# Performance work log

Measured on AMD Instinct MI355X. Metric: run time of the kernel, lower is better.

The kernel has to match this reference:

```python
import jax, jax.numpy as jnp
import numpy as np

N = 10000
E = 160000
IN_CH, HID, OUT = 14, 128, 4
HEADS = 8
NEG_SLOPE = 0.2


def setup_inputs() -> dict:
    key = jax.random.key(0)
    ks = jax.random.split(key, 16)
    glorot = lambda k, shape: jax.random.normal(k, shape, jnp.float32) * np.sqrt(2.0 / (shape[0] + shape[-1]))
    inp = {
        'x': jax.random.normal(ks[0], (N, IN_CH), jnp.float32),
        'edge_index': jax.random.randint(ks[1], (2, E), 0, N, jnp.int64),
        # layer 1: 14 -> 8 heads x 128, concat
        'W1': glorot(ks[2], (IN_CH, HEADS * HID)),
        'a_src1': glorot(ks[3], (HEADS, HID)),
        'a_dst1': glorot(ks[4], (HEADS, HID)),
        'b1': jnp.zeros((HEADS * HID,), jnp.float32),
        # layer 2: 1024 -> 8 heads x 128, concat
        'W2': glorot(ks[5], (HEADS * HID, HEADS * HID)),
        'a_src2': glorot(ks[6], (HEADS, HID)),
        'a_dst2': glorot(ks[7], (HEADS, HID)),
        'b2': jnp.zeros((HEADS * HID,), jnp.float32),
        # layer 3: 1024 -> 1 head x 4, mean (concat=False)
        'W3': glorot(ks[8], (HEADS * HID, OUT)),
        'a_src3': glorot(ks[9], (1, OUT)),
        'a_dst3': glorot(ks[10], (1, OUT)),
        'b3': jnp.zeros((OUT,), jnp.float32),
    }
    return inp


def gat_conv(x, src, dst, W, a_src, a_dst, b, heads, out_ch, concat):
    n = x.shape[0]
    h = (x @ W).reshape(n, heads, out_ch)                      # [N,H,C]
    al_s = jnp.sum(h * a_src, axis=-1)                         # [N,H]
    al_d = jnp.sum(h * a_dst, axis=-1)                         # [N,H]
    e = al_s[src] + al_d[dst]                                  # [E,H]
    e = jnp.where(e > 0, e, NEG_SLOPE * e)                     # LeakyReLU(0.2)
    # segment softmax over incoming edges of each dst node
    m = jax.ops.segment_max(e, dst, num_segments=n)
    ex = jnp.exp(e - m[dst])
    z = jax.ops.segment_sum(ex, dst, num_segments=n)
    alpha = ex / (z[dst] + 1e-16)                              # [E,H]
    out = jax.ops.segment_sum(h[src] * alpha[:, :, None], dst, num_segments=n)  # [N,H,C]
    out = out.reshape(n, heads * out_ch) if concat else out.mean(axis=1)
    return out + b


def reference(x, edge_index, W1, a_src1, a_dst1, b1, W2, a_src2, a_dst2, b2, W3, a_src3, a_dst3, b3):
    n = x.shape[0]
    # add self-loops (PyG GATConv default)
    loop = jnp.arange(n, dtype=edge_index.dtype)
    src = jnp.concatenate([edge_index[0], loop])
    dst = jnp.concatenate([edge_index[1], loop])
    # dropout layers are identity in eval mode
    h = gat_conv(x, src, dst, W1, a_src1, a_dst1, b1, HEADS, HID, True)
    h = jax.nn.relu(h)
    h = gat_conv(h, src, dst, W2, a_src2, a_dst2, b2, HEADS, HID, True)
    h = jax.nn.relu(h)
    h = gat_conv(h, src, dst, W3, a_src3, a_dst3, b3, 1, OUT, False)
    h = jax.nn.relu(h)
    return h
```

## Files before the change

kernel.cpp:

```cpp
#include <hip/hip_runtime.h>

typedef unsigned short ushort_t;
typedef unsigned int uint32;

#define N_NODES 10000
#define N_EDGES 160000
#define ET (N_NODES + N_EDGES)
#define HT 1024
#define HEADS 8
#define NEG 0.2f

#define O_FLAG     0
#define O_COUNTS   256
#define O_OFFS     (O_COUNTS + 40192)
#define O_SSORT    (O_OFFS + 40192)
#define O_ALS1     (O_SSORT + 680192)
#define O_ALD1     (O_ALS1 + 320000)
#define O_ALS2     (O_ALD1 + 320000)
#define O_ALD2     (O_ALS2 + 320000)
#define O_AL3S     O_ALS2
#define O_AL3D     (O_ALS2 + 40192)
#define O_H3       (O_ALS2 + 80384)
#define O_WVEC     (O_ALD2 + 320000)
#define O_W3F      (O_WVEC + 24576)
#define O_S3F      (O_W3F + 16384)
#define O_W2T      (O_S3F + 768)
#define O_BUFA     (O_W2T + 2097152)
#define O_BUFB     (O_BUFA + 20480000)

__device__ __forceinline__ float bf2f(ushort_t u){ return __uint_as_float(((uint32)u) << 16); }
__device__ __forceinline__ ushort_t f2bf(float f){
    uint32 x = __float_as_uint(f);
    return (ushort_t)((x + 0x7fffu + ((x >> 16) & 1u)) >> 16);
}
__device__ __forceinline__ void unpack2(uint32 u, float& lo, float& hi){
    lo = __uint_as_float(u << 16);
    hi = __uint_as_float(u & 0xffff0000u);
}

typedef __bf16 bf16x8 __attribute__((ext_vector_type(8)));
typedef float  f32x4  __attribute__((ext_vector_type(4)));

typedef const __attribute__((address_space(1))) uint32* gas1_u32;
typedef       __attribute__((address_space(3))) uint32* las3_u32;

__device__ __forceinline__ void gload_lds16(const void* g, void* l){
    __builtin_amdgcn_global_load_lds((gas1_u32)g, (las3_u32)l, 16, 0, 0);
}

__device__ __forceinline__ int probe_f32(const uint32* __restrict__ w){
    int cnt = 0;
    for (int i = 0; i < 256; i++){
        uint32 e = (w[i] >> 7) & 0xffu;
        cnt += (e >= 64u && e <= 160u) ? 1 : 0;
    }
    return (cnt > 200) ? 0 : 1;
}
__global__ void k_probe(const int* __restrict__ ei, const uint32* __restrict__ w1raw,
                        int* __restrict__ flags){
    if (threadIdx.x == 0){
        int nz = 0;
        for (int i = 0; i < 128; i++) nz |= ei[2*i + 1];
        flags[0] = (nz == 0) ? 1 : 0;
    }
    if (threadIdx.x == 1) flags[1] = probe_f32(w1raw);
}

__device__ __forceinline__ float cvt1(const void* p, int i, int f32){
    return f32 ? ((const float*)p)[i] : bf2f(((const ushort_t*)p)[i]);
}

struct CvtArgs {
    const void* vsrc[6];
    const void* w3src;
    const void* s3src[3];
};

__global__ __launch_bounds__(256) void k_setup(CvtArgs a, const void* __restrict__ W2,
                                               const int* __restrict__ flags,
                                               float* __restrict__ wvecF, float* __restrict__ W3F,
                                               float* __restrict__ s3F,
                                               int* __restrict__ counts,
                                               float* __restrict__ alS2, float* __restrict__ alD2,
                                               ushort_t* __restrict__ W2T){
    __shared__ ushort_t tile[32][33];
    int b = blockIdx.x, tid = threadIdx.x;
    int f32 = flags[1];
    if (b < 11){
        int g = b * 1024 + tid * 4;
        #pragma unroll
        for (int j = 0; j < 4; j++){
            int i = g + j;
            if (i < 6144) wvecF[i] = cvt1(a.vsrc[i >> 10], i & 1023, f32);
            else if (i < 10240) W3F[i - 6144] = cvt1(a.w3src, i - 6144, f32);
            else if (i < 10252){
                int off = i - 10240;
                s3F[(off >> 2) * 16 + (off & 3)] = cvt1(a.s3src[off >> 2], off & 3, f32);
            }
        }
    } else if (b < 21){
        int g = (b - 11) * 1024 + tid * 4;
        #pragma unroll
        for (int j = 0; j < 4; j++) if (g + j < N_NODES) counts[g + j] = 0;
    } else if (b < 178){
        int g = (b - 21) * 1024 + tid * 4;
        if (g < 80000){ *(float4*)(alS2 + g) = make_float4(0,0,0,0); }
        else if (g < 160000){ *(float4*)(alD2 + g - 80000) = make_float4(0,0,0,0); }
    } else {
        int t = b - 178;
        int bx = t & 31, by = t >> 5;
        int cx = tid & 31, ry = (tid >> 5) * 4;
        #pragma unroll
        for (int r = 0; r < 4; r++){
            size_t idx = (size_t)(by*32 + ry + r)*1024 + bx*32 + cx;
            tile[ry + r][cx] = f32 ? f2bf(((const float*)W2)[idx]) : ((const ushort_t*)W2)[idx];
        }
        __syncthreads();
        #pragma unroll
        for (int r = 0; r < 4; r++)
            W2T[(size_t)(bx*32 + ry + r)*1024 + by*32 + cx] = tile[cx][ry + r];
    }
}

__global__ __launch_bounds__(256) void k_extract_hist(const void* __restrict__ ei, const int* __restrict__ flags,
                                                      int* __restrict__ counts){
    int i = blockIdx.x * 256 + threadIdx.x;
    int is64 = flags[0];
    int d = -1;
    if (i < N_EDGES){
        d = is64 ? (int)((const long long*)ei)[N_EDGES + i] : ((const int*)ei)[N_EDGES + i];
    } else if (i < ET){
        d = i - N_EDGES;
    }
    if (d >= 0) atomicAdd(&counts[d], 1);
}

__global__ __launch_bounds__(1024) void k_scan(int* __restrict__ counts, int* __restrict__ offs, int n){
    __shared__ int wsum[16];
    __shared__ int running_s;
    int tid = threadIdx.x;
    int lane = tid & 63, wid = tid >> 6;
    if (tid == 0) running_s = 0;
    __syncthreads();
    for (int base = 0; base < n; base += 1024){
        int i = base + tid;
        int v = (i < n) ? counts[i] : 0;
        int x = v;
        #pragma unroll
        for (int d = 1; d < 64; d <<= 1){
            int t = __shfl_up(x, d, 64);
            if (lane >= d) x += t;
        }
        if (lane == 63) wsum[wid] = x;
        __syncthreads();
        if (wid == 0 && lane < 16){
            int w = wsum[lane];
            #pragma unroll
            for (int d = 1; d < 16; d <<= 1){
                int t = __shfl_up(w, d, 64);
                if (lane >= d) w += t;
            }
            wsum[lane] = w;
        }
        __syncthreads();
        int wprefix = (wid == 0) ? 0 : wsum[wid - 1];
        int run = running_s;
        int excl = run + wprefix + (x - v);
        if (i < n){ offs[i] = excl; counts[i] = excl; }
        __syncthreads();
        if (tid == 0) running_s = run + wsum[15];
        __syncthreads();
    }
    if (tid == 0) offs[n] = running_s;
}

__global__ __launch_bounds__(256) void k_scatter(const void* __restrict__ ei, const int* __restrict__ flags,
                                                 int* __restrict__ cursors, int* __restrict__ ssort){
    int i = blockIdx.x * 256 + threadIdx.x;
    if (i >= ET) return;
    int is64 = flags[0];
    int s, d;
    if (i < N_EDGES){
        if (is64){
            s = (int)((const long long*)ei)[i];
            d = (int)((const long long*)ei)[N_EDGES + i];
        } else {
            s = ((const int*)ei)[i];
            d = ((const int*)ei)[N_EDGES + i];
        }
    } else { s = i - N_EDGES; d = s; }
    int pos = atomicAdd(&cursors[d], 1);
    ssort[pos] = s;
}

__global__ __launch_bounds__(256) void k_gemm1f(const void* __restrict__ x, const void* __restrict__ W1,
                                                const int* __restrict__ flags,
                                                const float* __restrict__ wvecF,
                                                ushort_t* __restrict__ h1,
                                                float* __restrict__ alS, float* __restrict__ alD){
    __shared__ float w1s[14 * HT];
    int tid = threadIdx.x;
    int f32 = flags[1];
    if (f32){
        for (int i = tid * 4; i < 14 * HT; i += 1024)
            *(float4*)(w1s + i) = *(const float4*)((const float*)W1 + i);
    } else {
        for (int i = tid * 4; i < 14 * HT; i += 1024){
            uint2 u = *(const uint2*)((const ushort_t*)W1 + i);
            unpack2(u.x, w1s[i], w1s[i+1]);
            unpack2(u.y, w1s[i+2], w1s[i+3]);
        }
    }
    __syncthreads();
    int c0 = tid * 4;
    float4 sv = *(const float4*)(wvecF + c0);
    float4 dv = *(const float4*)(wvecF + 1024 + c0);
    int head = tid >> 5, l32 = tid & 31;
    #pragma unroll 1
    for (int n = blockIdx.x; n < N_NODES; n += 512){
        float a0=0.f, a1=0.f, a2=0.f, a3=0.f;
        #pragma unroll
        for (int k = 0; k < 14; k++){
            float xv = f32 ? ((const float*)x)[n*14 + k] : bf2f(((const ushort_t*)x)[n*14 + k]);
            float4 w = *(const float4*)(w1s + k*HT + c0);
            a0 += xv*w.x; a1 += xv*w.y; a2 += xv*w.z; a3 += xv*w.w;
        }
        uint2 o;
        o.x = (uint32)f2bf(a0) | ((uint32)f2bf(a1) << 16);
        o.y = (uint32)f2bf(a2) | ((uint32)f2bf(a3) << 16);
        *(uint2*)(h1 + (size_t)n*HT + c0) = o;
        float h0,h1v,h2,h3v;
        unpack2(o.x, h0, h1v); unpack2(o.y, h2, h3v);
        float s = h0*sv.x + h1v*sv.y + h2*sv.z + h3v*sv.w;
        float d = h0*dv.x + h1v*dv.y + h2*dv.z + h3v*dv.w;
        #pragma unroll
        for (int of = 16; of; of >>= 1){ s += __shfl_xor(s, of, 32); d += __shfl_xor(d, of, 32); }
        if (l32 == 0){ alS[n*HEADS + head] = s; alD[n*HEADS + head] = d; }
    }
}

__global__ __launch_bounds__(256) void k_gat_agg(const ushort_t* __restrict__ H, const float* __restrict__ alS,
                                                 const float* __restrict__ alD, const int* __restrict__ offs,
                                                 const int* __restrict__ srcs, const float* __restrict__ bias,
                                                 ushort_t* __restrict__ out){
    int tid = threadIdx.x;
    int wv = tid >> 6, lane = tid & 63;
    int n = blockIdx.x * 2 + (wv >> 1);
    int half = wv & 1;
    int beg = offs[n], end = offs[n+1];
    int head = half*4 + (lane >> 4);
    int slot = lane & 15;
    float ad = alD[n*HEADS + head];

    float m = -1e30f, z = 0.f;
    for (int c = beg; c < end; c += 64){
        int cn = min(64, end - c);
        int sreg = (lane < cn) ? srcs[c + lane] : 0;
        for (int p = slot; p < cn; p += 16){
            int s = __shfl(sreg, p, 64);
            float v = alS[s*HEADS + head] + ad;
            v = v > 0.f ? v : NEG*v;
            if (v > m){ z = z*__expf(m - v) + 1.f; m = v; }
            else z += __expf(v - m);
        }
    }
    #pragma unroll
    for (int o = 1; o < 16; o <<= 1){
        float m2 = __shfl_xor(m, o, 64);
        float z2 = __shfl_xor(z, o, 64);
        float nm = fmaxf(m, m2);
        z = z*__expf(m - nm) + z2*__expf(m2 - nm);
        m = nm;
    }
    float inv = 1.f / (z + 1e-16f);

    int ch0 = half*512 + lane*8;
    const ushort_t* Hc = H + ch0;
    float c0=0.f,c1=0.f,c2=0.f,c3=0.f,c4=0.f,c5=0.f,c6=0.f,c7=0.f;
    for (int c = beg; c < end; c += 64){
        int cn = min(64, end - c);
        int sreg = (lane < cn) ? srcs[c + lane] : 0;
        int j = 0;
        for (; j + 8 <= cn; j += 8){
            int s[8]; uint4 u[8]; float w[8];
            #pragma unroll
            for (int q = 0; q < 8; q++) s[q] = __shfl(sreg, j + q, 64);
            #pragma unroll
            for (int q = 0; q < 8; q++) u[q] = *(const uint4*)(Hc + (size_t)s[q]*HT);
            #pragma unroll
            for (int q = 0; q < 8; q++){
                float v = alS[s[q]*HEADS + head] + ad;
                v = v > 0.f ? v : NEG*v;
                w[q] = __expf(v - m) * inv;
            }
            #pragma unroll
            for (int q = 0; q < 8; q++){
                float f0,f1,f2,f3,f4,f5,f6,f7;
                unpack2(u[q].x,f0,f1); unpack2(u[q].y,f2,f3);
                unpack2(u[q].z,f4,f5); unpack2(u[q].w,f6,f7);
                c0+=w[q]*f0; c1+=w[q]*f1; c2+=w[q]*f2; c3+=w[q]*f3;
                c4+=w[q]*f4; c5+=w[q]*f5; c6+=w[q]*f6; c7+=w[q]*f7;
            }
        }
        for (; j < cn; j++){
            int s0 = __shfl(sreg, j, 64);
            uint4 u0 = *(const uint4*)(Hc + (size_t)s0*HT);
            float v0 = alS[s0*HEADS + head] + ad;
            v0 = v0 > 0.f ? v0 : NEG*v0;
            float w0 = __expf(v0 - m) * inv;
            float f0,f1,f2,f3,f4,f5,f6,f7;
            unpack2(u0.x,f0,f1); unpack2(u0.y,f2,f3); unpack2(u0.z,f4,f5); unpack2(u0.w,f6,f7);
            c0+=w0*f0; c1+=w0*f1; c2+=w0*f2; c3+=w0*f3;
            c4+=w0*f4; c5+=w0*f5; c6+=w0*f6; c7+=w0*f7;
        }
    }
    float4 b0 = *(const float4*)(bias + ch0);
    float4 b1 = *(const float4*)(bias + ch0 + 4);
    c0 = fmaxf(c0+b0.x, 0.f); c1 = fmaxf(c1+b0.y, 0.f);
    c2 = fmaxf(c2+b0.z, 0.f); c3 = fmaxf(c3+b0.w, 0.f);
    c4 = fmaxf(c4+b1.x, 0.f); c5 = fmaxf(c5+b1.y, 0.f);
    c6 = fmaxf(c6+b1.z, 0.f); c7 = fmaxf(c7+b1.w, 0.f);
    uint4 o;
    o.x = (uint32)f2bf(c0) | ((uint32)f2bf(c1) << 16);
    o.y = (uint32)f2bf(c2) | ((uint32)f2bf(c3) << 16);
    o.z = (uint32)f2bf(c4) | ((uint32)f2bf(c5) << 16);
    o.w = (uint32)f2bf(c6) | ((uint32)f2bf(c7) << 16);
    *(uint4*)(out + (size_t)n*HT + ch0) = o;
}

__global__ __launch_bounds__(256) void k_gemm2(const ushort_t* __restrict__ A, const ushort_t* __restrict__ BT,
                                               ushort_t* __restrict__ C,
                                               const float* __restrict__ aS, const float* __restrict__ aD,
                                               float* __restrict__ alS2, float* __restrict__ alD2){
    __shared__ ushort_t lA[128*32];
    __shared__ ushort_t lB[64*32];
    int bn = blockIdx.x, bm = blockIdx.y;
    int tid = threadIdx.x;
    int lane = tid & 63;
    int wave = tid >> 6;
    int wm = wave * 32;
    int lm = lane & 15, kg = lane >> 4;
    f32x4 acc[2][4];
    #pragma unroll
    for (int i = 0; i < 2; i++)
        #pragma unroll
        for (int j = 0; j < 4; j++) acc[i][j] = (f32x4)0.0f;

    int rowA0 = bm * 128, rowB0 = bn * 64;
    for (int k0 = 0; k0 < 1024; k0 += 32){
        #pragma unroll
        for (int it = 0; it < 2; ++it){
            int s = tid + it*256;
            int r = s >> 2, q = s & 3;
            int ra = rowA0 + r; if (ra > N_NODES-1) ra = N_NODES-1;
            gload_lds16(A + (size_t)ra*1024 + k0 + q*8, lA + s*8);
        }
        {
            int r = tid >> 2, q = tid & 3;
            gload_lds16(BT + (size_t)(rowB0 + r)*1024 + k0 + q*8, lB + tid*8);
        }
        __syncthreads();
        bf16x8 af[2], bfr[4];
        #pragma unroll
        for (int mt = 0; mt < 2; mt++) af[mt]  = *(const bf16x8*)(lA + (wm + mt*16 + lm)*32 + kg*8);
        #pragma unroll
        for (int nt = 0; nt < 4; nt++) bfr[nt] = *(const bf16x8*)(lB + (nt*16 + lm)*32 + kg*8);
        #pragma unroll
        for (int mt = 0; mt < 2; mt++)
            #pragma unroll
            for (int nt = 0; nt < 4; nt++)
                acc[mt][nt] = __builtin_amdgcn_mfma_f32_16x16x32_bf16(af[mt], bfr[nt], acc[mt][nt], 0, 0, 0);
        __syncthreads();
    }
    #pragma unroll
    for (int mt = 0; mt < 2; mt++){
        int row_base = bm*128 + wm + mt*16 + kg*4;
        #pragma unroll
        for (int nt = 0; nt < 4; nt++){
            int col = bn*64 + nt*16 + lm;
            #pragma unroll
            for (int r = 0; r < 4; r++){
                int row = row_base + r;
                if (row < N_NODES) C[(size_t)row*HT + col] = f2bf(acc[mt][nt][r]);
            }
        }
    }
    int head = bn >> 1;
    float as_l[4], ad_l[4];
    #pragma unroll
    for (int nt = 0; nt < 4; nt++){
        as_l[nt] = aS[bn*64 + nt*16 + lm];
        ad_l[nt] = aD[bn*64 + nt*16 + lm];
    }
    #pragma unroll
    for (int mt = 0; mt < 2; mt++){
        #pragma unroll
        for (int r = 0; r < 4; r++){
            float ps = acc[mt][0][r]*as_l[0] + acc[mt][1][r]*as_l[1]
                     + acc[mt][2][r]*as_l[2] + acc[mt][3][r]*as_l[3];
            float pd = acc[mt][0][r]*ad_l[0] + acc[mt][1][r]*ad_l[1]
                     + acc[mt][2][r]*ad_l[2] + acc[mt][3][r]*ad_l[3];
            #pragma unroll
            for (int o = 1; o < 16; o <<= 1){ ps += __shfl_xor(ps, o, 64); pd += __shfl_xor(pd, o, 64); }
            if (lm == 0){
                int row = bm*128 + wm + mt*16 + kg*4 + r;
                if (row < N_NODES){
                    atomicAdd(&alS2[row*HEADS + head], ps);
                    atomicAdd(&alD2[row*HEADS + head], pd);
                }
            }
        }
    }
}

__global__ __launch_bounds__(256) void k_gemm3(const ushort_t* __restrict__ A, const float* __restrict__ W3,
                                               const float* __restrict__ s3,
                                               float* __restrict__ h3, float* __restrict__ al3s, float* __restrict__ al3d){
    int tid = threadIdx.x;
    int lane = tid & 63, wave = tid >> 6;
    int n = blockIdx.x * 4 + wave;
    if (n >= N_NODES) return;
    float4 w3r[16];
    #pragma unroll
    for (int j = 0; j < 16; j++) w3r[j] = ((const float4*)W3)[lane*16 + j];
    const uint4* ap = (const uint4*)(A + (size_t)n*HT + lane*16);
    uint4 u0 = ap[0], u1 = ap[1];
    uint32 uu[8] = {u0.x,u0.y,u0.z,u0.w,u1.x,u1.y,u1.z,u1.w};
    float acc0=0.f, acc1=0.f, acc2=0.f, acc3=0.f;
    #pragma unroll
    for (int p = 0; p < 8; p++){
        float lo, hi;
        unpack2(uu[p], lo, hi);
        float4 wl = w3r[p*2], wh = w3r[p*2+1];
        acc0 += lo*wl.x + hi*wh.x;
        acc1 += lo*wl.y + hi*wh.y;
        acc2 += lo*wl.z + hi*wh.z;
        acc3 += lo*wl.w + hi*wh.w;
    }
    #pragma unroll
    for (int o = 32; o; o >>= 1){
        acc0 += __shfl_xor(acc0, o, 64); acc1 += __shfl_xor(acc1, o, 64);
        acc2 += __shfl_xor(acc2, o, 64); acc3 += __shfl_xor(acc3, o, 64);
    }
    if (lane == 0){
        *(float4*)(h3 + n*4) = make_float4(acc0, acc1, acc2, acc3);
        al3s[n] = acc0*s3[0] + acc1*s3[1] + acc2*s3[2] + acc3*s3[3];
        al3d[n] = acc0*s3[16] + acc1*s3[17] + acc2*s3[18] + acc3*s3[19];
    }
}

__global__ __launch_bounds__(256) void k_gat_agg3(const float* __restrict__ h3, const float* __restrict__ al3s,
                                                  const float* __restrict__ al3d, const int* __restrict__ offs,
                                                  const int* __restrict__ srcs, const float* __restrict__ b3,
                                                  const int* __restrict__ flags, void* __restrict__ out){
    int tid = threadIdx.x;
    int l = tid & 63, wave = tid >> 6;
    int n = blockIdx.x * 4 + wave;
    if (n >= N_NODES) return;
    int beg = offs[n], end = offs[n+1];
    float ad = al3d[n];
    float m = -1e30f;
    for (int e = beg + l; e < end; e += 64){
        float v = al3s[srcs[e]] + ad; v = v > 0.f ? v : NEG*v;
        m = fmaxf(m, v);
    }
    #pragma unroll
    for (int o = 32; o; o >>= 1) m = fmaxf(m, __shfl_xor(m, o, 64));
    float z = 0.f;
    for (int e = beg + l; e < end; e += 64){
        float v = al3s[srcs[e]] + ad; v = v > 0.f ? v : NEG*v;
        z += __expf(v - m);
    }
    #pragma unroll
    for (int o = 32; o; o >>= 1) z += __shfl_xor(z, o, 64);
    float inv = 1.f / (z + 1e-16f);
    float a0=0.f, a1=0.f, a2=0.f, a3=0.f;
    for (int e = beg + l; e < end; e += 64){
        int s = srcs[e];
        float v = al3s[s] + ad; v = v > 0.f ? v : NEG*v;
        float w = __expf(v - m) * inv;
        float4 hv = *(const float4*)(h3 + s*4);
        a0 += w*hv.x; a1 += w*hv.y; a2 += w*hv.z; a3 += w*hv.w;
    }
    #pragma unroll
    for (int o = 32; o; o >>= 1){
        a0 += __shfl_xor(a0, o, 64); a1 += __shfl_xor(a1, o, 64);
        a2 += __shfl_xor(a2, o, 64); a3 += __shfl_xor(a3, o, 64);
    }
    if (l == 0){
        float r0 = fmaxf(a0 + b3[0], 0.f);
        float r1 = fmaxf(a1 + b3[1], 0.f);
        float r2 = fmaxf(a2 + b3[2], 0.f);
        float r3 = fmaxf(a3 + b3[3], 0.f);
        if (flags[1]){
            float* o4 = (float*)out;
            o4[n*4+0]=r0; o4[n*4+1]=r1; o4[n*4+2]=r2; o4[n*4+3]=r3;
        } else {
            ushort_t* o2 = (ushort_t*)out;
            o2[n*4+0]=f2bf(r0); o2[n*4+1]=f2bf(r1); o2[n*4+2]=f2bf(r2); o2[n*4+3]=f2bf(r3);
        }
    }
}

extern "C" void kernel_launch(void* const* d_in, const int* in_sizes, int n_in,
                              void* d_out, int out_size, void* d_ws, size_t ws_size,
                              hipStream_t stream){
    const void* x   = d_in[0];
    const void* ei  = d_in[1];
    const void* W1  = d_in[2];
    const void* W2  = d_in[6];
    const void* W3  = d_in[10];

    char* ws = (char*)d_ws;
    int* flags     = (int*)(ws + O_FLAG);
    int* counts    = (int*)(ws + O_COUNTS);
    int* offs      = (int*)(ws + O_OFFS);
    int* ssort     = (int*)(ws + O_SSORT);
    float* alS1    = (float*)(ws + O_ALS1);
    float* alD1    = (float*)(ws + O_ALD1);
    float* alS2    = (float*)(ws + O_ALS2);
    float* alD2    = (float*)(ws + O_ALD2);
    float* al3s    = (float*)(ws + O_AL3S);
    float* al3d    = (float*)(ws + O_AL3D);
    float* h3      = (float*)(ws + O_H3);
    float* wvecF   = (float*)(ws + O_WVEC);
    float* W3F     = (float*)(ws + O_W3F);
    float* s3F     = (float*)(ws + O_S3F);
    ushort_t* W2T  = (ushort_t*)(ws + O_W2T);
    ushort_t* bufA = (ushort_t*)(ws + O_BUFA);
    ushort_t* bufB = (ushort_t*)(ws + O_BUFB);

    const int EB = (ET + 255) / 256;

    CvtArgs ca;
    ca.vsrc[0]=d_in[3];  ca.vsrc[1]=d_in[4];  ca.vsrc[2]=d_in[5];
    ca.vsrc[3]=d_in[7];  ca.vsrc[4]=d_in[8];  ca.vsrc[5]=d_in[9];
    ca.w3src = W3;
    ca.s3src[0]=d_in[11]; ca.s3src[1]=d_in[12]; ca.s3src[2]=d_in[13];

    k_probe<<<1, 64, 0, stream>>>((const int*)ei, (const uint32*)W1, flags);
    k_setup<<<1202, 256, 0, stream>>>(ca, W2, flags, wvecF, W3F, s3F, counts, alS2, alD2, W2T);
    k_extract_hist<<<EB, 256, 0, stream>>>(ei, flags, counts);
    k_scan<<<1, 1024, 0, stream>>>(counts, offs, N_NODES);
    k_scatter<<<EB, 256, 0, stream>>>(ei, flags, counts, ssort);

    k_gemm1f<<<512, 256, 0, stream>>>(x, W1, flags, wvecF, bufA, alS1, alD1);
    k_gat_agg<<<5000, 256, 0, stream>>>(bufA, alS1, alD1, offs, ssort, wvecF + 2*1024, bufB);

    k_gemm2<<<dim3(16, 79), 256, 0, stream>>>(bufB, W2T, bufA, wvecF + 3*1024, wvecF + 4*1024, alS2, alD2);
    k_gat_agg<<<5000, 256, 0, stream>>>(bufA, alS2, alD2, offs, ssort, wvecF + 5*1024, bufB);

    k_gemm3<<<2500, 256, 0, stream>>>(bufB, W3F, s3F, h3, al3s, al3d);
    k_gat_agg3<<<2500, 256, 0, stream>>>(h3, al3s, al3d, offs, ssort, s3F + 32, flags, d_out);
}
```

Before: 358.3 us.

## Replace per-node softmax max pass with global bound; widen GEMM2 K-tile with swizzle

The aggregation kernel drops its first pass over each node's edges, which computed the online softmax max and sum. Instead it subtracts a global upper bound on the attention logits, built as per-head atomic maxima of the nonnegative parts of the source and destination scores, and normalizes once at the end. A new small kernel computes that bound for layer 2, and GEMM1 computes it for layer 1. GEMM2 also moves to 64-wide K tiles with an XOR-swizzled LDS layout, which halves the number of barrier iterations and is meant to reduce bank conflicts. The bound trick risks exp underflow when a node's logits sit far below the global maximum.

```diff
diff --git a/kernel.cpp b/kernel.cpp
--- a/kernel.cpp
+++ b/kernel.cpp
@@ -11,6 +11,7 @@
 #define NEG 0.2f
 
 #define O_FLAG     0
+#define O_BND      64
 #define O_COUNTS   256
 #define O_OFFS     (O_COUNTS + 40192)
 #define O_SSORT    (O_OFFS + 40192)
@@ -82,11 +83,13 @@
                                                float* __restrict__ s3F,
                                                int* __restrict__ counts,
                                                float* __restrict__ alS2, float* __restrict__ alD2,
+                                               uint32* __restrict__ bnd,
                                                ushort_t* __restrict__ W2T){
     __shared__ ushort_t tile[32][33];
     int b = blockIdx.x, tid = threadIdx.x;
     int f32 = flags[1];
     if (b < 11){
+        if (b == 0 && tid < 32) bnd[tid] = 0;
         int g = b * 1024 + tid * 4;
         #pragma unroll
         for (int j = 0; j < 4; j++){
@@ -197,10 +200,13 @@
                                                 const int* __restrict__ flags,
                                                 const float* __restrict__ wvecF,
                                                 ushort_t* __restrict__ h1,
-                                                float* __restrict__ alS, float* __restrict__ alD){
+                                                float* __restrict__ alS, float* __restrict__ alD,
+                                                uint32* __restrict__ bnd){
     __shared__ float w1s[14 * HT];
+    __shared__ uint32 smax[16];
     int tid = threadIdx.x;
     int f32 = flags[1];
+    if (tid < 16) smax[tid] = 0;
     if (f32){
         for (int i = tid * 4; i < 14 * HT; i += 1024)
             *(float4*)(w1s + i) = *(const float4*)((const float*)W1 + i);
@@ -235,12 +241,36 @@
         float d = h0*dv.x + h1v*dv.y + h2*dv.z + h3v*dv.w;
         #pragma unroll
         for (int of = 16; of; of >>= 1){ s += __shfl_xor(s, of, 32); d += __shfl_xor(d, of, 32); }
-        if (l32 == 0){ alS[n*HEADS + head] = s; alD[n*HEADS + head] = d; }
+        if (l32 == 0){
+            alS[n*HEADS + head] = s; alD[n*HEADS + head] = d;
+            atomicMax(&smax[head],     __float_as_uint(fmaxf(s, 0.f)));
+            atomicMax(&smax[8 + head], __float_as_uint(fmaxf(d, 0.f)));
+        }
+    }
+    __syncthreads();
+    if (tid < 16) atomicMax(&bnd[tid], smax[tid]);
+}
+
+__global__ __launch_bounds__(256) void k_bound(const float* __restrict__ alS2, const float* __restrict__ alD2,
+                                               uint32* __restrict__ bnd){
+    int g = blockIdx.x * 256 + threadIdx.x;
+    int lane = threadIdx.x & 63;
+    float ms = 0.f, md = 0.f;
+    for (int i = g; i < 80000; i += 10240){ ms = fmaxf(ms, alS2[i]); md = fmaxf(md, alD2[i]); }
+    #pragma unroll
+    for (int o = 8; o < 64; o <<= 1){
+        ms = fmaxf(ms, __shfl_xor(ms, o, 64));
+        md = fmaxf(md, __shfl_xor(md, o, 64));
+    }
+    if (lane < 8){
+        atomicMax(&bnd[16 + lane], __float_as_uint(ms));
+        atomicMax(&bnd[24 + lane], __float_as_uint(md));
     }
 }
 
 __global__ __launch_bounds__(256) void k_gat_agg(const ushort_t* __restrict__ H, const float* __restrict__ alS,
-                                                 const float* __restrict__ alD, const int* __restrict__ offs,
+                                                 const float* __restrict__ alD, const uint32* __restrict__ bnd,
+                                                 int bo, const int* __restrict__ offs,
                                                  const int* __restrict__ srcs, const float* __restrict__ bias,
                                                  ushort_t* __restrict__ out){
     int tid = threadIdx.x;
@@ -249,77 +279,58 @@
     int half = wv & 1;
     int beg = offs[n], end = offs[n+1];
     int head = half*4 + (lane >> 4);
-    int slot = lane & 15;
     float ad = alD[n*HEADS + head];
-
-    float m = -1e30f, z = 0.f;
-    for (int c = beg; c < end; c += 64){
-        int cn = min(64, end - c);
-        int sreg = (lane < cn) ? srcs[c + lane] : 0;
-        for (int p = slot; p < cn; p += 16){
-            int s = __shfl(sreg, p, 64);
-            float v = alS[s*HEADS + head] + ad;
-            v = v > 0.f ? v : NEG*v;
-            if (v > m){ z = z*__expf(m - v) + 1.f; m = v; }
-            else z += __expf(v - m);
-        }
-    }
-    #pragma unroll
-    for (int o = 1; o < 16; o <<= 1){
-        float m2 = __shfl_xor(m, o, 64);
-        float z2 = __shfl_xor(z, o, 64);
-        float nm = fmaxf(m, m2);
-        z = z*__expf(m - nm) + z2*__expf(m2 - nm);
-        m = nm;
-    }
-    float inv = 1.f / (z + 1e-16f);
+    float B = __uint_as_float(bnd[bo + head]) + __uint_as_float(bnd[bo + 8 + head]);
 
     int ch0 = half*512 + lane*8;
     const ushort_t* Hc = H + ch0;
+    float z = 0.f;
     float c0=0.f,c1=0.f,c2=0.f,c3=0.f,c4=0.f,c5=0.f,c6=0.f,c7=0.f;
     for (int c = beg; c < end; c += 64){
         int cn = min(64, end - c);
         int sreg = (lane < cn) ? srcs[c + lane] : 0;
         int j = 0;
         for (; j + 8 <= cn; j += 8){
-            int s[8]; uint4 u[8]; float w[8];
+            int s[8]; uint4 u[8]; float e[8];
             #pragma unroll
             for (int q = 0; q < 8; q++) s[q] = __shfl(sreg, j + q, 64);
             #pragma unroll
             for (int q = 0; q < 8; q++) u[q] = *(const uint4*)(Hc + (size_t)s[q]*HT);
             #pragma unroll
+            for (int q = 0; q < 8; q++) e[q] = alS[s[q]*HEADS + head];
+            #pragma unroll
             for (int q = 0; q < 8; q++){
-                float v = alS[s[q]*HEADS + head] + ad;
+                float v = e[q] + ad;
                 v = v > 0.f ? v : NEG*v;
-                w[q] = __expf(v - m) * inv;
-            }
-            #pragma unroll
-            for (int q = 0; q < 8; q++){
+                float w = __expf(v - B);
+                z += w;
                 float f0,f1,f2,f3,f4,f5,f6,f7;
                 unpack2(u[q].x,f0,f1); unpack2(u[q].y,f2,f3);
                 unpack2(u[q].z,f4,f5); unpack2(u[q].w,f6,f7);
-                c0+=w[q]*f0; c1+=w[q]*f1; c2+=w[q]*f2; c3+=w[q]*f3;
-                c4+=w[q]*f4; c5+=w[q]*f5; c6+=w[q]*f6; c7+=w[q]*f7;
+                c0+=w*f0; c1+=w*f1; c2+=w*f2; c3+=w*f3;
+                c4+=w*f4; c5+=w*f5; c6+=w*f6; c7+=w*f7;
             }
         }
         for (; j < cn; j++){
             int s0 = __shfl(sreg, j, 64);
             uint4 u0 = *(const uint4*)(Hc + (size_t)s0*HT);
-            float v0 = alS[s0*HEADS + head] + ad;
-            v0 = v0 > 0.f ? v0 : NEG*v0;
-            float w0 = __expf(v0 - m) * inv;
+            float v = alS[s0*HEADS + head] + ad;
+            v = v > 0.f ? v : NEG*v;
+            float w = __expf(v - B);
+            z += w;
             float f0,f1,f2,f3,f4,f5,f6,f7;
             unpack2(u0.x,f0,f1); unpack2(u0.y,f2,f3); unpack2(u0.z,f4,f5); unpack2(u0.w,f6,f7);
-            c0+=w0*f0; c1+=w0*f1; c2+=w0*f2; c3+=w0*f3;
-            c4+=w0*f4; c5+=w0*f5; c6+=w0*f6; c7+=w0*f7;
-        }
-    }
+            c0+=w*f0; c1+=w*f1; c2+=w*f2; c3+=w*f3;
+            c4+=w*f4; c5+=w*f5; c6+=w*f6; c7+=w*f7;
+        }
+    }
+    float inv = 1.f / z;
     float4 b0 = *(const float4*)(bias + ch0);
     float4 b1 = *(const float4*)(bias + ch0 + 4);
-    c0 = fmaxf(c0+b0.x, 0.f); c1 = fmaxf(c1+b0.y, 0.f);
-    c2 = fmaxf(c2+b0.z, 0.f); c3 = fmaxf(c3+b0.w, 0.f);
-    c4 = fmaxf(c4+b1.x, 0.f); c5 = fmaxf(c5+b1.y, 0.f);
-    c6 = fmaxf(c6+b1.z, 0.f); c7 = fmaxf(c7+b1.w, 0.f);
+    c0 = fmaxf(c0*inv + b0.x, 0.f); c1 = fmaxf(c1*inv + b0.y, 0.f);
+    c2 = fmaxf(c2*inv + b0.z, 0.f); c3 = fmaxf(c3*inv + b0.w, 0.f);
+    c4 = fmaxf(c4*inv + b1.x, 0.f); c5 = fmaxf(c5*inv + b1.y, 0.f);
+    c6 = fmaxf(c6*inv + b1.z, 0.f); c7 = fmaxf(c7*inv + b1.w, 0.f);
     uint4 o;
     o.x = (uint32)f2bf(c0) | ((uint32)f2bf(c1) << 16);
     o.y = (uint32)f2bf(c2) | ((uint32)f2bf(c3) << 16);
@@ -332,14 +343,15 @@
                                                ushort_t* __restrict__ C,
                                                const float* __restrict__ aS, const float* __restrict__ aD,
                                                float* __restrict__ alS2, float* __restrict__ alD2){
-    __shared__ ushort_t lA[128*32];
-    __shared__ ushort_t lB[64*32];
+    __shared__ ushort_t lA[128*64];
+    __shared__ ushort_t lB[64*64];
     int bn = blockIdx.x, bm = blockIdx.y;
     int tid = threadIdx.x;
     int lane = tid & 63;
     int wave = tid >> 6;
     int wm = wave * 32;
     int lm = lane & 15, kg = lane >> 4;
+    int swz = lm & 7;
     f32x4 acc[2][4];
     #pragma unroll
     for (int i = 0; i < 2; i++)
@@ -347,29 +359,36 @@
         for (int j = 0; j < 4; j++) acc[i][j] = (f32x4)0.0f;
 
     int rowA0 = bm * 128, rowB0 = bn * 64;
-    for (int k0 = 0; k0 < 1024; k0 += 32){
+    for (int k0 = 0; k0 < 1024; k0 += 64){
+        #pragma unroll
+        for (int it = 0; it < 4; ++it){
+            int s = tid + it*256;
+            int r = s >> 3, q = s & 7;
+            int ra = rowA0 + r; if (ra > N_NODES-1) ra = N_NODES-1;
+            gload_lds16(A + (size_t)ra*1024 + k0 + (q ^ (r & 7))*8, lA + s*8);
+        }
         #pragma unroll
         for (int it = 0; it < 2; ++it){
             int s = tid + it*256;
-            int r = s >> 2, q = s & 3;
-            int ra = rowA0 + r; if (ra > N_NODES-1) ra = N_NODES-1;
-            gload_lds16(A + (size_t)ra*1024 + k0 + q*8, lA + s*8);
-        }
-        {
-            int r = tid >> 2, q = tid & 3;
-            gload_lds16(BT + (size_t)(rowB0 + r)*1024 + k0 + q*8, lB + tid*8);
-        }
-        __syncthreads();
-        bf16x8 af[2], bfr[4];
-        #pragma unroll
-        for (int mt = 0; mt < 2; mt++) af[mt]  = *(const bf16x8*)(lA + (wm + mt*16 + lm)*32 + kg*8);
-        #pragma unroll
-        for (int nt = 0; nt < 4; nt++) bfr[nt] = *(const bf16x8*)(lB + (nt*16 + lm)*32 + kg*8);
-        #pragma unroll
-        for (int mt = 0; mt < 2; mt++)
-            #pragma unroll
-            for (int nt = 0; nt < 4; nt++)
-                acc[mt][nt] = __builtin_amdgcn_mfma_f32_16x16x32_bf16(af[mt], bfr[nt], acc[mt][nt], 0, 0, 0);
+            int r = s >> 3, q = s & 7;
+            gload_lds16(BT + (size_t)(rowB0 + r)*1024 + k0 + (q ^ (r & 7))*8, lB + s*8);
+        }
+        __syncthreads();
+        #pragma unroll
+        for (int kh = 0; kh < 2; kh++){
+            bf16x8 af[2], bfr[4];
+            int qb = kh*4 + kg;
+            int qp = (qb ^ swz) * 8;
+            #pragma unroll
+            for (int mt = 0; mt < 2; mt++) af[mt]  = *(const bf16x8*)(lA + (wm + mt*16 + lm)*64 + qp);
+            #pragma unroll
+            for (int nt = 0; nt < 4; nt++) bfr[nt] = *(const bf16x8*)(lB + (nt*16 + lm)*64 + qp);
+            #pragma unroll
+            for (int mt = 0; mt < 2; mt++)
+                #pragma unroll
+                for (int nt = 0; nt < 4; nt++)
+                    acc[mt][nt] = __builtin_amdgcn_mfma_f32_16x16x32_bf16(af[mt], bfr[nt], acc[mt][nt], 0, 0, 0);
+        }
         __syncthreads();
     }
     #pragma unroll
@@ -513,6 +532,7 @@
 
     char* ws = (char*)d_ws;
     int* flags     = (int*)(ws + O_FLAG);
+    uint32* bnd    = (uint32*)(ws + O_BND);
     int* counts    = (int*)(ws + O_COUNTS);
     int* offs      = (int*)(ws + O_OFFS);
     int* ssort     = (int*)(ws + O_SSORT);
@@ -539,16 +559,17 @@
     ca.s3src[0]=d_in[11]; ca.s3src[1]=d_in[12]; ca.s3src[2]=d_in[13];
 
     k_probe<<<1, 64, 0, stream>>>((const int*)ei, (const uint32*)W1, flags);
-    k_setup<<<1202, 256, 0, stream>>>(ca, W2, flags, wvecF, W3F, s3F, counts, alS2, alD2, W2T);
+    k_setup<<<1202, 256, 0, stream>>>(ca, W2, flags, wvecF, W3F, s3F, counts, alS2, alD2, bnd, W2T);
     k_extract_hist<<<EB, 256, 0, stream>>>(ei, flags, counts);
     k_scan<<<1, 1024, 0, stream>>>(counts, offs, N_NODES);
     k_scatter<<<EB, 256, 0, stream>>>(ei, flags, counts, ssort);
 
-    k_gemm1f<<<512, 256, 0, stream>>>(x, W1, flags, wvecF, bufA, alS1, alD1);
-    k_gat_agg<<<5000, 256, 0, stream>>>(bufA, alS1, alD1, offs, ssort, wvecF + 2*1024, bufB);
+    k_gemm1f<<<512, 256, 0, stream>>>(x, W1, flags, wvecF, bufA, alS1, alD1, bnd);
+    k_gat_agg<<<5000, 256, 0, stream>>>(bufA, alS1, alD1, bnd, 0, offs, ssort, wvecF + 2*1024, bufB);
 
     k_gemm2<<<dim3(16, 79), 256, 0, stream>>>(bufB, W2T, bufA, wvecF + 3*1024, wvecF + 4*1024, alS2, alD2);
-    k_gat_agg<<<5000, 256, 0, stream>>>(bufA, alS2, alD2, offs, ssort, wvecF + 5*1024, bufB);
+    k_bound<<<40, 256, 0, stream>>>(alS2, alD2, bnd);
+    k_gat_agg<<<5000, 256, 0, stream>>>(bufA, alS2, alD2, bnd, 16, offs, ssort, wvecF + 5*1024, bufB);
 
     k_gemm3<<<2500, 256, 0, stream>>>(bufB, W3F, s3F, h3, al3s, al3d);
     k_gat_agg3<<<2500, 256, 0, stream>>>(h3, al3s, al3d, offs, ssort, s3F + 32, flags, d_out);
```

New measurement: 342.4 us. 4.4% less time.
